# Optimization experiments

Measured on AMD Instinct MI355X. Metric: run time of the kernel, lower is better.

The kernel has to match this reference:

```python
import jax, jax.numpy as jnp
import numpy as np

N, D, H, E = 4096, 512, 8, 131072
DH = D // H
EPS = 1e-5
NEG = -1e9


def layer_norm(x, w, b):
    m = jnp.mean(x, axis=-1, keepdims=True)
    v = jnp.mean((x - m) ** 2, axis=-1, keepdims=True)
    return (x - m) * jax.lax.rsqrt(v + EPS) * w + b


def setup_inputs() -> dict:
    key = jax.random.key(0)
    ks = jax.random.split(key, 10)
    s = 0.02
    return {
        "x": jax.random.normal(ks[0], (N, D), dtype=jnp.float32),
        "edge_index": jax.random.randint(ks[1], (2, E), 0, N, dtype=jnp.int64),
        "ln1_w": jnp.ones((D,), jnp.float32),
        "ln1_b": jnp.zeros((D,), jnp.float32),
        "w_in": jax.random.normal(ks[2], (3 * D, D), jnp.float32) * s,
        "b_in": jnp.zeros((3 * D,), jnp.float32),
        "w_out": jax.random.normal(ks[3], (D, D), jnp.float32) * s,
        "b_out": jnp.zeros((D,), jnp.float32),
        "ln2_w": jnp.ones((D,), jnp.float32),
        "ln2_b": jnp.zeros((D,), jnp.float32),
        "w1": jax.random.normal(ks[4], (4 * D, D), jnp.float32) * s,
        "b1": jnp.zeros((4 * D,), jnp.float32),
        "w2": jax.random.normal(ks[5], (D, 4 * D), jnp.float32) * s,
        "b2": jnp.zeros((D,), jnp.float32),
    }


def reference(x, edge_index, ln1_w, ln1_b, w_in, b_in, w_out, b_out,
              ln2_w, ln2_b, w1, b1, w2, b2):
    n = x.shape[0]
    # adjacency mask: allowed where edge exists or on diagonal
    adj = jnp.zeros((n, n), dtype=bool)
    adj = adj.at[edge_index[0], edge_index[1]].set(True)
    adj = adj.at[jnp.arange(n), jnp.arange(n)].set(True)
    add_mask = jnp.where(adj, 0.0, NEG).astype(x.dtype)  # [n, n]

    xn = layer_norm(x, ln1_w, ln1_b)
    qkv = xn @ w_in.T + b_in  # [n, 3D]
    q, k, v = jnp.split(qkv, 3, axis=-1)
    # [n, D] -> [H, n, DH]
    q = q.reshape(n, H, DH).transpose(1, 0, 2)
    k = k.reshape(n, H, DH).transpose(1, 0, 2)
    v = v.reshape(n, H, DH).transpose(1, 0, 2)
    scores = jnp.einsum("hqd,hkd->hqk", q, k) / jnp.sqrt(jnp.asarray(DH, x.dtype))
    scores = scores + add_mask[None]
    attn = jax.nn.softmax(scores, axis=-1)
    o = jnp.einsum("hqk,hkd->hqd", attn, v)  # [H, n, DH]
    o = o.transpose(1, 0, 2).reshape(n, D)
    attn_out = o @ w_out.T + b_out

    x = x + attn_out  # residual (dropout=0 / eval)
    xm = layer_norm(x, ln2_w, ln2_b)
    mlp = jax.nn.relu(xm @ w1.T + b1) @ w2.T + b2
    return x + mlp
```

## Files before the change

### kernel.cpp

```cpp
#include <hip/hip_runtime.h>

#define NN 4096
#define DD 512
#define HH 8
#define DHH 64

typedef __attribute__((ext_vector_type(8))) __bf16 bfrag;
typedef __attribute__((ext_vector_type(8))) short short8;
typedef __attribute__((ext_vector_type(8))) unsigned short ushort8v;
typedef __attribute__((ext_vector_type(4))) float f32x4;
typedef unsigned int uint32;

#define GLOAD16(gp, lp)                                                        \
    __builtin_amdgcn_global_load_lds(                                          \
        (const __attribute__((address_space(1))) unsigned int*)(gp),           \
        (__attribute__((address_space(3))) unsigned int*)(lp), 16, 0, 0)

template <int N>
__device__ __forceinline__ void waitcnt_vm() {
    if constexpr (N == 0) asm volatile("s_waitcnt vmcnt(0)" ::: "memory");
    else if constexpr (N == 4) asm volatile("s_waitcnt vmcnt(4)" ::: "memory");
    else if constexpr (N == 6) asm volatile("s_waitcnt vmcnt(6)" ::: "memory");
    else if constexpr (N == 8) asm volatile("s_waitcnt vmcnt(8)" ::: "memory");
    else if constexpr (N == 12) asm volatile("s_waitcnt vmcnt(12)" ::: "memory");
    else static_assert(N == 0, "unsupported vmcnt literal");
}

__device__ __forceinline__ unsigned short f2b(float f) {
    unsigned int u = __builtin_bit_cast(unsigned int, f);
    unsigned int r = 0x7fffu + ((u >> 16) & 1u);
    return (unsigned short)((u + r) >> 16);
}

__device__ __forceinline__ float b2f(unsigned short u) {
    return __builtin_bit_cast(float, (unsigned int)u << 16);
}

__device__ __forceinline__ float fexp2(float x) {
#if __has_builtin(__builtin_amdgcn_exp2f)
    return __builtin_amdgcn_exp2f(x);
#else
    return exp2f(x);
#endif
}

__device__ __forceinline__ void load_edge(const void* ei, int E, int i, int is32,
                                          int& r, int& c) {
    if (is32) {
        const int* p = (const int*)ei;
        r = p[i]; c = p[E + i];
    } else {
        const long long* p = (const long long*)ei;
        r = (int)p[i]; c = (int)p[E + i];
    }
}

__device__ __forceinline__ void ln_row_wave(const float* __restrict__ x,
                                            const float* __restrict__ w,
                                            const float* __restrict__ b,
                                            unsigned short* __restrict__ out,
                                            int row, int lane) {
    const float4* xp = reinterpret_cast<const float4*>(x + (size_t)row * DD + lane * 8);
    const float4 v0 = xp[0], v1 = xp[1];
    float s  = (v0.x + v0.y) + (v0.z + v0.w) + (v1.x + v1.y) + (v1.z + v1.w);
    float s2 = v0.x * v0.x + v0.y * v0.y + v0.z * v0.z + v0.w * v0.w +
               v1.x * v1.x + v1.y * v1.y + v1.z * v1.z + v1.w * v1.w;
#pragma unroll
    for (int d = 1; d < 64; d <<= 1) {
        s += __shfl_xor(s, d);
        s2 += __shfl_xor(s2, d);
    }
    const float mean = s * (1.f / DD);
    const float var = fmaxf(s2 * (1.f / DD) - mean * mean, 0.f);
    const float rs = rsqrtf(var + 1e-5f);
    const float4* wp = reinterpret_cast<const float4*>(w + lane * 8);
    const float4* bp = reinterpret_cast<const float4*>(b + lane * 8);
    const float4 w0 = wp[0], w1 = wp[1], b0 = bp[0], b1 = bp[1];
    ushort8v o;
    o[0] = f2b((v0.x - mean) * rs * w0.x + b0.x);
    o[1] = f2b((v0.y - mean) * rs * w0.y + b0.y);
    o[2] = f2b((v0.z - mean) * rs * w0.z + b0.z);
    o[3] = f2b((v0.w - mean) * rs * w0.w + b0.w);
    o[4] = f2b((v1.x - mean) * rs * w1.x + b1.x);
    o[5] = f2b((v1.y - mean) * rs * w1.y + b1.y);
    o[6] = f2b((v1.z - mean) * rs * w1.z + b1.z);
    o[7] = f2b((v1.w - mean) * rs * w1.w + b1.w);
    *reinterpret_cast<ushort8v*>(out + (size_t)row * DD + lane * 8) = o;
}

__global__ __launch_bounds__(256) void ln_rows(const float* __restrict__ x,
                                               const float* __restrict__ w,
                                               const float* __restrict__ b,
                                               unsigned short* __restrict__ out) {
    ln_row_wave(x, w, b, out, blockIdx.x * 4 + (threadIdx.x >> 6), threadIdx.x & 63);
}

#define W_IN_N 786432
#define W_OUT_N 262144
#define W1_N 1048576
#define W2_N 1048576
#define CVT_BLKS 3072
#define LN_BLKS 1024
__global__ __launch_bounds__(256) void prologue(
    const float* __restrict__ w_in, const float* __restrict__ w_out,
    const float* __restrict__ w1, const float* __restrict__ w2,
    unsigned short* __restrict__ o_in, unsigned short* __restrict__ o_out,
    unsigned short* __restrict__ o1, unsigned short* __restrict__ o2,
    const float* __restrict__ x, const float* __restrict__ ln1w,
    const float* __restrict__ ln1b, unsigned short* __restrict__ xn,
    const void* __restrict__ ei, uint32* __restrict__ mask, int E) {
    const int bb = blockIdx.x;
    if (bb < CVT_BLKS) {
        int idx = (bb * 256 + threadIdx.x) * 4;
        const float* src;
        unsigned short* dst;
        int off;
        if (idx < W_IN_N) { src = w_in; dst = o_in; off = idx; }
        else if (idx < W_IN_N + W_OUT_N) { src = w_out; dst = o_out; off = idx - W_IN_N; }
        else if (idx < W_IN_N + W_OUT_N + W1_N) { src = w1; dst = o1; off = idx - (W_IN_N + W_OUT_N); }
        else { src = w2; dst = o2; off = idx - (W_IN_N + W_OUT_N + W1_N); }
        float4 v = *reinterpret_cast<const float4*>(src + off);
        ushort4 o;
        o.x = f2b(v.x); o.y = f2b(v.y); o.z = f2b(v.z); o.w = f2b(v.w);
        *reinterpret_cast<ushort4*>(dst + off) = o;
    } else if (bb < CVT_BLKS + LN_BLKS) {
        ln_row_wave(x, ln1w, ln1b, xn,
                    (bb - CVT_BLKS) * 4 + (threadIdx.x >> 6), threadIdx.x & 63);
    } else {
        __shared__ int s_any;
        if (threadIdx.x == 0) s_any = 0;
        __syncthreads();
        if (((const int*)ei)[2 * threadIdx.x + 1] != 0) atomicOr(&s_any, 1);
        __syncthreads();
        const int is32 = s_any;
        const int tid = (bb - (CVT_BLKS + LN_BLKS)) * 256 + threadIdx.x;
        const int total = E + NN;
        if (tid < total) {
            int r, c;
            if (tid < E) load_edge(ei, E, tid, is32, r, c);
            else { r = tid - E; c = r; }
            atomicOr(&mask[r * 128 + (c >> 5)], 1u << (c & 31));
        }
    }
}

template <int BM, int BN, int EPI>
__global__ __launch_bounds__(256) void gemm_swz(const unsigned short* __restrict__ A,
                                                const unsigned short* __restrict__ B,
                                                int K,
                                                const float* __restrict__ bias,
                                                const float* __restrict__ resid,
                                                float* __restrict__ out_f,
                                                unsigned short* __restrict__ out_b,
                                                unsigned short* __restrict__ q_out,
                                                unsigned short* __restrict__ k_out,
                                                unsigned short* __restrict__ v_out) {
    constexpr int MR = BM / 32;
    constexpr int NR = BN / 32;
    constexpr int LA = BM / 32;
    constexpr int LB = BN / 32;
    constexpr int CSTR = BN + 4;
    constexpr size_t PIPE_B = (size_t)2 * (BM + BN) * 64 * 2;
    constexpr size_t EPI_B = (size_t)BM * CSTR * 4;
    constexpr size_t LDS_B = PIPE_B > EPI_B ? PIPE_B : EPI_B;
    __shared__ __align__(16) unsigned char smem[LDS_B];
    unsigned short* a_lds = (unsigned short*)smem;
    unsigned short* b_lds = a_lds + (size_t)2 * BM * 64;
    float* c_lds = (float*)smem;

    const int tid = threadIdx.x;
    const int lane = tid & 63;
    const int wave = tid >> 6;
    const int wm = wave >> 1, wn = wave & 1;
    const int wgid = blockIdx.x;
    const int tm = wgid % (NN / BM);
    const int tn = wgid / (NN / BM);

    f32x4 acc[MR][NR];
#pragma unroll
    for (int mi = 0; mi < MR; ++mi)
#pragma unroll
        for (int ni = 0; ni < NR; ++ni) acc[mi][ni] = (f32x4){0.f, 0.f, 0.f, 0.f};

    const int srow = lane >> 3;
    const int sswz = ((lane & 7) ^ srow) << 3;
    const unsigned short* a_src = A + (size_t)(tm * BM + srow) * K + sswz;
    const unsigned short* b_src = B + (size_t)(tn * BN + srow) * K + sswz;

    auto stage = [&](int k0, int buf) {
        unsigned short* al = a_lds + buf * (BM * 64);
        unsigned short* bl = b_lds + buf * (BN * 64);
#pragma unroll
        for (int i = 0; i < LA; ++i) {
            const int c = wave * LA + i;
            GLOAD16(a_src + (size_t)c * 8 * K + k0, al + c * 512);
        }
#pragma unroll
        for (int i = 0; i < LB; ++i) {
            const int c = wave * LB + i;
            GLOAD16(b_src + (size_t)c * 8 * K + k0, bl + c * 512);
        }
    };

    const int NT = K >> 6;
    stage(0, 0);
    for (int t = 0; t < NT; ++t) {
        const int cur = t & 1;
        if (t + 1 < NT) {
            stage((t + 1) << 6, cur ^ 1);
            waitcnt_vm<LA + LB>();
        } else {
            waitcnt_vm<0>();
        }
        __builtin_amdgcn_s_barrier();
        asm volatile("" ::: "memory");
        const unsigned short* al = a_lds + cur * (BM * 64);
        const unsigned short* bl = b_lds + cur * (BN * 64);
#pragma unroll
        for (int ks = 0; ks < 2; ++ks) {
            const int cswz = (((lane >> 4) + ks * 4) ^ (lane & 7)) << 3;
            const int rl = lane & 15;
            bfrag af[MR], bfr[NR];
#pragma unroll
            for (int mi = 0; mi < MR; ++mi)
                af[mi] = *reinterpret_cast<const bfrag*>(
                    &al[(wm * (BM / 2) + mi * 16 + rl) * 64 + cswz]);
#pragma unroll
            for (int ni = 0; ni < NR; ++ni)
                bfr[ni] = *reinterpret_cast<const bfrag*>(
                    &bl[(wn * (BN / 2) + ni * 16 + rl) * 64 + cswz]);
#pragma unroll
            for (int mi = 0; mi < MR; ++mi)
#pragma unroll
                for (int ni = 0; ni < NR; ++ni)
                    acc[mi][ni] = __builtin_amdgcn_mfma_f32_16x16x32_bf16(
                        af[mi], bfr[ni], acc[mi][ni], 0, 0, 0);
        }
        asm volatile("" ::: "memory");
        __builtin_amdgcn_s_barrier();
    }

    __syncthreads();
    {
        const int r0 = (lane >> 4) << 2;
        const int cl = lane & 15;
        float bias_r[NR];
#pragma unroll
        for (int ni = 0; ni < NR; ++ni)
            bias_r[ni] = bias[tn * BN + wn * (BN / 2) + ni * 16 + cl];
#pragma unroll
        for (int mi = 0; mi < MR; ++mi)
#pragma unroll
            for (int ni = 0; ni < NR; ++ni) {
                const int row_l = wm * (BM / 2) + mi * 16 + r0;
                const int col_l = wn * (BN / 2) + ni * 16 + cl;
#pragma unroll
                for (int r = 0; r < 4; ++r)
                    c_lds[(size_t)(row_l + r) * CSTR + col_l] =
                        acc[mi][ni][r] + bias_r[ni];
            }
    }
    __syncthreads();

    if constexpr (EPI == 1) {
        constexpr int IT = (BM * BN) / 1024;
#pragma unroll
        for (int it = 0; it < IT; ++it) {
            const int seg = tid + it * 256;
            const int row = seg / (BN / 4);
            const int c4 = (seg % (BN / 4)) * 4;
            f32x4 v = *reinterpret_cast<const f32x4*>(&c_lds[(size_t)row * CSTR + c4]);
            const size_t gidx = (size_t)(tm * BM + row) * 512 + tn * BN + c4;
            f32x4 rs = *reinterpret_cast<const f32x4*>(&resid[gidx]);
            *reinterpret_cast<f32x4*>(&out_f[gidx]) = v + rs;
        }
    } else {
        constexpr int IT = (BM * BN) / 2048;
        unsigned short* dst;
        int cbase, stride;
        float scl = 1.f;
        if constexpr (EPI == 0) {
            const int gc0 = tn * BN;
            const int region = gc0 >> 9;
            dst = region == 0 ? q_out : (region == 1 ? k_out : v_out);
            cbase = gc0 - region * 512;
            stride = 512;
            if (region == 0) scl = 0.18033688011112042f;
        } else {
            dst = out_b;
            cbase = tn * BN;
            stride = 2048;
        }
#pragma unroll
        for (int it = 0; it < IT; ++it) {
            const int seg = tid + it * 256;
            const int row = seg / (BN / 8);
            const int c8 = (seg % (BN / 8)) * 8;
            f32x4 v0 = *reinterpret_cast<const f32x4*>(&c_lds[(size_t)row * CSTR + c8]);
            f32x4 v1 = *reinterpret_cast<const f32x4*>(&c_lds[(size_t)row * CSTR + c8 + 4]);
            ushort8v o;
            if constexpr (EPI == 0) {
#pragma unroll
                for (int i = 0; i < 4; ++i) o[i] = f2b(v0[i] * scl);
#pragma unroll
                for (int i = 0; i < 4; ++i) o[4 + i] = f2b(v1[i] * scl);
            } else {
#pragma unroll
                for (int i = 0; i < 4; ++i) o[i] = f2b(fmaxf(v0[i], 0.f));
#pragma unroll
                for (int i = 0; i < 4; ++i) o[4 + i] = f2b(fmaxf(v1[i], 0.f));
            }
            *reinterpret_cast<ushort8v*>(
                dst + (size_t)(tm * BM + row) * stride + cbase + c8) = o;
        }
    }
}

__global__ __launch_bounds__(256) void attn_sparse(const unsigned short* __restrict__ qb,
                                                   const unsigned short* __restrict__ kb,
                                                   const unsigned short* __restrict__ vb,
                                                   const uint32* __restrict__ mask,
                                                   unsigned short* __restrict__ o_buf) {
    __shared__ int s_cols[4][1024];
    __shared__ int s_cnt[4];
    const int lane = threadIdx.x & 63;
    const int wid = threadIdx.x >> 6;
    const int q = blockIdx.x * 4 + wid;

    if (lane == 0) s_cnt[wid] = 0;
    uint32 w0 = mask[q * 128 + lane];
    uint32 w1 = mask[q * 128 + 64 + lane];
    const int base0 = lane * 32, base1 = (64 + lane) * 32;
    while (w0) {
        int b = __builtin_ctz(w0);
        w0 &= w0 - 1;
        int pos = atomicAdd(&s_cnt[wid], 1);
        s_cols[wid][pos & 1023] = base0 + b;
    }
    while (w1) {
        int b = __builtin_ctz(w1);
        w1 &= w1 - 1;
        int pos = atomicAdd(&s_cnt[wid], 1);
        s_cols[wid][pos & 1023] = base1 + b;
    }
    const int cnt = min(s_cnt[wid], 1024);

    ushort8v q8 = *reinterpret_cast<const ushort8v*>(qb + (size_t)q * DD + lane * 8);
    float qf[8];
#pragma unroll
    for (int i = 0; i < 8; ++i) qf[i] = b2f(q8[i]);

    float m_run = -3.0e38f, l_run = 0.f;
    float oa[8];
#pragma unroll
    for (int i = 0; i < 8; ++i) oa[i] = 0.f;

    for (int j0 = 0; j0 < cnt; j0 += 8) {
        float s_arr[8];
        int col_arr[8];
#pragma unroll
        for (int u = 0; u < 8; ++u) {
            const int idx = j0 + u;
            const bool act = idx < cnt;
            const int col = s_cols[wid][act ? idx : 0];
            col_arr[u] = col;
            ushort8v kq = *reinterpret_cast<const ushort8v*>(
                kb + (size_t)col * DD + lane * 8);
            float d = qf[0] * b2f(kq[0]);
            d = fmaf(qf[1], b2f(kq[1]), d);
            d = fmaf(qf[2], b2f(kq[2]), d);
            d = fmaf(qf[3], b2f(kq[3]), d);
            d = fmaf(qf[4], b2f(kq[4]), d);
            d = fmaf(qf[5], b2f(kq[5]), d);
            d = fmaf(qf[6], b2f(kq[6]), d);
            d = fmaf(qf[7], b2f(kq[7]), d);
            d += __shfl_xor(d, 1);
            d += __shfl_xor(d, 2);
            d += __shfl_xor(d, 4);
            s_arr[u] = act ? d : -3.0e38f;
        }
        float mloc = fmaxf(fmaxf(fmaxf(s_arr[0], s_arr[1]), fmaxf(s_arr[2], s_arr[3])),
                           fmaxf(fmaxf(s_arr[4], s_arr[5]), fmaxf(s_arr[6], s_arr[7])));
        if (mloc > m_run) {
            const float alpha = fexp2(m_run - mloc);
            l_run *= alpha;
#pragma unroll
            for (int i = 0; i < 8; ++i) oa[i] *= alpha;
            m_run = mloc;
        }
#pragma unroll
        for (int u = 0; u < 8; ++u) {
            const float p = fexp2(s_arr[u] - m_run);
            l_run += p;
            ushort8v vq = *reinterpret_cast<const ushort8v*>(
                vb + (size_t)col_arr[u] * DD + lane * 8);
#pragma unroll
            for (int i = 0; i < 8; ++i) oa[i] = fmaf(p, b2f(vq[i]), oa[i]);
        }
    }

    const float rl = 1.f / l_run;
    ushort8v ov;
#pragma unroll
    for (int i = 0; i < 8; ++i) ov[i] = f2b(oa[i] * rl);
    *reinterpret_cast<ushort8v*>(o_buf + (size_t)q * DD + lane * 8) = ov;
}

extern "C" void kernel_launch(void* const* d_in, const int* in_sizes, int n_in,
                              void* d_out, int out_size, void* d_ws, size_t ws_size,
                              hipStream_t stream) {
    const float* x = (const float*)d_in[0];
    const void* ei = d_in[1];
    const float* ln1w = (const float*)d_in[2];
    const float* ln1b = (const float*)d_in[3];
    const float* w_in = (const float*)d_in[4];
    const float* b_in = (const float*)d_in[5];
    const float* w_out = (const float*)d_in[6];
    const float* b_out = (const float*)d_in[7];
    const float* ln2w = (const float*)d_in[8];
    const float* ln2b = (const float*)d_in[9];
    const float* w1 = (const float*)d_in[10];
    const float* b1 = (const float*)d_in[11];
    const float* w2 = (const float*)d_in[12];
    const float* b2 = (const float*)d_in[13];
    float* out = (float*)d_out;
    const int E = in_sizes[1] / 2;

    char* ws = (char*)d_ws;
    size_t off = 0;
    auto alloc = [&](size_t bytes) -> void* {
        void* p = ws + off;
        off = (off + bytes + 255) & ~(size_t)255;
        return p;
    };
    uint32* mask1 = (uint32*)alloc((size_t)NN * 128 * 4);
    unsigned short* w_in_b = (unsigned short*)alloc((size_t)1536 * 512 * 2);
    unsigned short* w_out_b = (unsigned short*)alloc((size_t)512 * 512 * 2);
    unsigned short* w1_b = (unsigned short*)alloc((size_t)2048 * 512 * 2);
    unsigned short* w2_b = (unsigned short*)alloc((size_t)512 * 2048 * 2);
    unsigned short* xn = (unsigned short*)alloc((size_t)NN * DD * 2);
    unsigned short* q_b = (unsigned short*)alloc((size_t)NN * DD * 2);
    unsigned short* k_b = (unsigned short*)alloc((size_t)NN * DD * 2);
    unsigned short* v_b = (unsigned short*)alloc((size_t)NN * DD * 2);
    unsigned short* o_buf = (unsigned short*)alloc((size_t)NN * DD * 2);
    float* x1 = (float*)alloc((size_t)NN * DD * 4);
    unsigned short* xm = (unsigned short*)alloc((size_t)NN * DD * 2);
    unsigned short* h_buf = q_b;

    hipMemsetAsync(mask1, 0, (size_t)NN * 128 * 4, stream);

    const int adj_blks = (E + NN + 255) / 256;
    prologue<<<CVT_BLKS + LN_BLKS + adj_blks, 256, 0, stream>>>(
        w_in, w_out, w1, w2, w_in_b, w_out_b, w1_b, w2_b,
        x, ln1w, ln1b, xn, ei, mask1, E);

    gemm_swz<128, 64, 0><<<32 * 24, 256, 0, stream>>>(
        xn, w_in_b, 512, b_in, nullptr, nullptr, nullptr, q_b, k_b, v_b);
    attn_sparse<<<NN / 4, 256, 0, stream>>>(q_b, k_b, v_b, mask1, o_buf);
    gemm_swz<64, 64, 1><<<64 * 8, 256, 0, stream>>>(
        o_buf, w_out_b, 512, b_out, x, x1, nullptr, nullptr, nullptr, nullptr);
    ln_rows<<<NN / 4, 256, 0, stream>>>(x1, ln2w, ln2b, xm);
    gemm_swz<128, 128, 2><<<32 * 16, 256, 0, stream>>>(
        xm, w1_b, 512, b1, nullptr, nullptr, h_buf, nullptr, nullptr, nullptr);
    gemm_swz<64, 64, 1><<<64 * 8, 256, 0, stream>>>(
        h_buf, w2_b, 2048, b2, x1, out, nullptr, nullptr, nullptr, nullptr);
}
```

Baseline: 97.41 us.

## Fuse mask zeroing, adjacency build and LN2 into neighbouring kernels

Replaces the memset with zeroing blocks inside the prologue, moves the edge-to-bitmask atomic scatter into the start of the QKV GEMM, and folds the second layer norm into the out-projection GEMM epilogue. In that epilogue the last column tile of each row strip, detected with an atomic counter, normalises the strip. This removes one memset and one standalone kernel launch and shortens the prologue. The cost is extra atomic work ahead of the QKV GEMM main loop and a serialized LN tail run by only the finishing block of each row strip.

```diff
diff --git a/kernel.cpp b/kernel.cpp
--- a/kernel.cpp
+++ b/kernel.cpp
@@ -88,19 +88,13 @@
     *reinterpret_cast<ushort8v*>(out + (size_t)row * DD + lane * 8) = o;
 }
 
-__global__ __launch_bounds__(256) void ln_rows(const float* __restrict__ x,
-                                               const float* __restrict__ w,
-                                               const float* __restrict__ b,
-                                               unsigned short* __restrict__ out) {
-    ln_row_wave(x, w, b, out, blockIdx.x * 4 + (threadIdx.x >> 6), threadIdx.x & 63);
-}
-
 #define W_IN_N 786432
 #define W_OUT_N 262144
 #define W1_N 1048576
 #define W2_N 1048576
 #define CVT_BLKS 3072
 #define LN_BLKS 1024
+#define ZERO_BLKS 32
 __global__ __launch_bounds__(256) void prologue(
     const float* __restrict__ w_in, const float* __restrict__ w_out,
     const float* __restrict__ w1, const float* __restrict__ w2,
@@ -108,7 +102,7 @@
     unsigned short* __restrict__ o1, unsigned short* __restrict__ o2,
     const float* __restrict__ x, const float* __restrict__ ln1w,
     const float* __restrict__ ln1b, unsigned short* __restrict__ xn,
-    const void* __restrict__ ei, uint32* __restrict__ mask, int E) {
+    uint32* __restrict__ mask, uint32* __restrict__ row_cnt) {
     const int bb = blockIdx.x;
     if (bb < CVT_BLKS) {
         int idx = (bb * 256 + threadIdx.x) * 4;
@@ -127,20 +121,13 @@
         ln_row_wave(x, ln1w, ln1b, xn,
                     (bb - CVT_BLKS) * 4 + (threadIdx.x >> 6), threadIdx.x & 63);
     } else {
-        __shared__ int s_any;
-        if (threadIdx.x == 0) s_any = 0;
-        __syncthreads();
-        if (((const int*)ei)[2 * threadIdx.x + 1] != 0) atomicOr(&s_any, 1);
-        __syncthreads();
-        const int is32 = s_any;
-        const int tid = (bb - (CVT_BLKS + LN_BLKS)) * 256 + threadIdx.x;
-        const int total = E + NN;
-        if (tid < total) {
-            int r, c;
-            if (tid < E) load_edge(ei, E, tid, is32, r, c);
-            else { r = tid - E; c = r; }
-            atomicOr(&mask[r * 128 + (c >> 5)], 1u << (c & 31));
-        }
+        const int z = bb - (CVT_BLKS + LN_BLKS);
+        uint4 zero4 = {0u, 0u, 0u, 0u};
+        uint4* mp = reinterpret_cast<uint4*>(mask);
+#pragma unroll
+        for (int i = 0; i < 16; ++i)
+            mp[(size_t)z * 4096 + i * 256 + threadIdx.x] = zero4;
+        if (z == 0 && threadIdx.x < 64) row_cnt[threadIdx.x] = 0u;
     }
 }
 
@@ -154,7 +141,13 @@
                                                 unsigned short* __restrict__ out_b,
                                                 unsigned short* __restrict__ q_out,
                                                 unsigned short* __restrict__ k_out,
-                                                unsigned short* __restrict__ v_out) {
+                                                unsigned short* __restrict__ v_out,
+                                                const void* __restrict__ ei,
+                                                uint32* __restrict__ mask, int E,
+                                                const float* __restrict__ ln2w,
+                                                const float* __restrict__ ln2b,
+                                                unsigned short* __restrict__ xm_out,
+                                                uint32* __restrict__ row_cnt) {
     constexpr int MR = BM / 32;
     constexpr int NR = BN / 32;
     constexpr int LA = BM / 32;
@@ -176,6 +169,20 @@
     const int tm = wgid % (NN / BM);
     const int tn = wgid / (NN / BM);
 
+    if constexpr (EPI == 0) {
+        if (mask) {
+            const int odd = ((const int*)ei)[2 * lane + 1];
+            const int is32 = (__ballot(odd != 0) != 0ull) ? 1 : 0;
+            const int total = E + NN;
+            for (int i = wgid * 256 + tid; i < total; i += (int)gridDim.x * 256) {
+                int r, c;
+                if (i < E) load_edge(ei, E, i, is32, r, c);
+                else { r = i - E; c = r; }
+                atomicOr(&mask[r * 128 + (c >> 5)], 1u << (c & 31));
+            }
+        }
+    }
+
     f32x4 acc[MR][NR];
 #pragma unroll
     for (int mi = 0; mi < MR; ++mi)
@@ -273,6 +280,22 @@
             const size_t gidx = (size_t)(tm * BM + row) * 512 + tn * BN + c4;
             f32x4 rs = *reinterpret_cast<const f32x4*>(&resid[gidx]);
             *reinterpret_cast<f32x4*>(&out_f[gidx]) = v + rs;
+        }
+        if (row_cnt) {
+            constexpr int NCOL = 512 / BN;
+            __shared__ int s_last;
+            __threadfence();
+            __syncthreads();
+            if (tid == 0) {
+                uint32 old = atomicAdd(&row_cnt[tm], 1u);
+                s_last = (old == NCOL - 1);
+            }
+            __syncthreads();
+            if (s_last) {
+                __threadfence();
+                for (int r = wave; r < BM; r += 4)
+                    ln_row_wave(out_f, ln2w, ln2b, xm_out, tm * BM + r, lane);
+            }
         }
     } else {
         constexpr int IT = (BM * BN) / 2048;
@@ -434,6 +457,7 @@
         return p;
     };
     uint32* mask1 = (uint32*)alloc((size_t)NN * 128 * 4);
+    uint32* row_cnt = (uint32*)alloc(64 * 4);
     unsigned short* w_in_b = (unsigned short*)alloc((size_t)1536 * 512 * 2);
     unsigned short* w_out_b = (unsigned short*)alloc((size_t)512 * 512 * 2);
     unsigned short* w1_b = (unsigned short*)alloc((size_t)2048 * 512 * 2);
@@ -447,21 +471,25 @@
     unsigned short* xm = (unsigned short*)alloc((size_t)NN * DD * 2);
     unsigned short* h_buf = q_b;
 
-    hipMemsetAsync(mask1, 0, (size_t)NN * 128 * 4, stream);
-
-    const int adj_blks = (E + NN + 255) / 256;
-    prologue<<<CVT_BLKS + LN_BLKS + adj_blks, 256, 0, stream>>>(
+    prologue<<<CVT_BLKS + LN_BLKS + ZERO_BLKS, 256, 0, stream>>>(
         w_in, w_out, w1, w2, w_in_b, w_out_b, w1_b, w2_b,
-        x, ln1w, ln1b, xn, ei, mask1, E);
+        x, ln1w, ln1b, xn, mask1, row_cnt);
 
     gemm_swz<128, 64, 0><<<32 * 24, 256, 0, stream>>>(
-        xn, w_in_b, 512, b_in, nullptr, nullptr, nullptr, q_b, k_b, v_b);
+        xn, w_in_b, 512, b_in, nullptr, nullptr, nullptr, q_b, k_b, v_b,
+        ei, mask1, E, nullptr, nullptr, nullptr, nullptr);
+
     attn_sparse<<<NN / 4, 256, 0, stream>>>(q_b, k_b, v_b, mask1, o_buf);
+
     gemm_swz<64, 64, 1><<<64 * 8, 256, 0, stream>>>(
-        o_buf, w_out_b, 512, b_out, x, x1, nullptr, nullptr, nullptr, nullptr);
-    ln_rows<<<NN / 4, 256, 0, stream>>>(x1, ln2w, ln2b, xm);
+        o_buf, w_out_b, 512, b_out, x, x1, nullptr, nullptr, nullptr, nullptr,
+        nullptr, nullptr, 0, ln2w, ln2b, xm, row_cnt);
+
     gemm_swz<128, 128, 2><<<32 * 16, 256, 0, stream>>>(
-        xm, w1_b, 512, b1, nullptr, nullptr, h_buf, nullptr, nullptr, nullptr);
+        xm, w1_b, 512, b1, nullptr, nullptr, h_buf, nullptr, nullptr, nullptr,
+        nullptr, nullptr, 0, nullptr, nullptr, nullptr, nullptr);
+
     gemm_swz<64, 64, 1><<<64 * 8, 256, 0, stream>>>(
-        h_buf, w2_b, 2048, b2, x1, out, nullptr, nullptr, nullptr, nullptr);
-}
+        h_buf, w2_b, 2048, b2, x1, out, nullptr, nullptr, nullptr, nullptr,
+        nullptr, nullptr, 0, nullptr, nullptr, nullptr, nullptr);
+}
```

Result: slower. 166.9 us (+71.4%).
